# Kernel tuning notes

Hardware: AMD Instinct MI355X
Metric: run time of the kernel (lower is better)

Reference implementation:

```python
import jax, jax.numpy as jnp
import numpy as np

DMODEL = 1024
HEADS = 16
HEAD_SIZE = DMODEL // HEADS


def setup_inputs() -> dict:
    key = jax.random.key(0)
    ks = jax.random.split(key, 9)
    s = 1.0 / np.sqrt(DMODEL)
    x = jax.random.normal(ks[0], (4, 2048, DMODEL), dtype=jnp.float32)
    Wq = jax.random.uniform(ks[1], (DMODEL, DMODEL), jnp.float32, -s, s)
    bq = jax.random.uniform(ks[2], (DMODEL,), jnp.float32, -s, s)
    Wk = jax.random.uniform(ks[3], (DMODEL, DMODEL), jnp.float32, -s, s)
    bk = jax.random.uniform(ks[4], (DMODEL,), jnp.float32, -s, s)
    Wv = jax.random.uniform(ks[5], (DMODEL, DMODEL), jnp.float32, -s, s)
    bv = jax.random.uniform(ks[6], (DMODEL,), jnp.float32, -s, s)
    Wo = jax.random.uniform(ks[7], (DMODEL, DMODEL), jnp.float32, -s, s)
    bo = jax.random.uniform(ks[8], (DMODEL,), jnp.float32, -s, s)
    return {"x": x, "Wq": Wq, "bq": bq, "Wk": Wk, "bk": bk,
            "Wv": Wv, "bv": bv, "Wo": Wo, "bo": bo}


def _split_heads(t):
    b, s, _ = t.shape
    return t.reshape(b, s, HEADS, HEAD_SIZE).transpose(0, 2, 1, 3)  # [b,h,s,d]


def reference(x, Wq, bq, Wk, bk, Wv, bv, Wo, bo):
    q = _split_heads(x @ Wq.T + bq)
    k = _split_heads(x @ Wk.T + bk)
    v = _split_heads(x @ Wv.T + bv)
    scale = 1.0 / jnp.sqrt(jnp.float32(HEAD_SIZE))
    scores = jnp.einsum("bhqd,bhkd->bhqk", q, k) * scale  # full [B,H,S,S]
    attn = jax.nn.softmax(scores, axis=-1)
    out = jnp.einsum("bhqk,bhkd->bhqd", attn, v)
    b, h, s, d = out.shape
    out = out.transpose(0, 2, 1, 3).reshape(b, s, h * d)
    return out @ Wo.T + bo
```

## Files before the change

kernel.cpp:

```cpp
#include <hip/hip_runtime.h>

typedef _Float16 f16x8 __attribute__((ext_vector_type(8)));
typedef _Float16 f16x4 __attribute__((ext_vector_type(4)));
typedef float f32x4 __attribute__((ext_vector_type(4)));
typedef unsigned u32x2 __attribute__((ext_vector_type(2)));

#define MFMA16(a, b, c) __builtin_amdgcn_mfma_f32_16x16x32_f16(a, b, c, 0, 0, 0)

static constexpr int DM   = 1024;
static constexpr int SEQ  = 2048;
static constexpr int NHEAD = 16;
static constexpr int HD   = 64;

#if __has_builtin(__builtin_amdgcn_exp2f) && \
    __has_builtin(__builtin_amdgcn_permlane32_swap) && \
    __has_builtin(__builtin_amdgcn_permlane16_swap)
#define SAFE_CHAIN 1
#else
#define SAFE_CHAIN 0
#endif

__device__ __forceinline__ float fexp2(float x) {
#if SAFE_CHAIN
  return __builtin_amdgcn_exp2f(x);
#else
  float y; asm("v_exp_f32 %0, %1" : "=v"(y) : "v"(x)); return y;
#endif
}

__device__ __forceinline__ void plswap2(unsigned& x, unsigned& y) {
#if SAFE_CHAIN
  u32x2 r = __builtin_amdgcn_permlane32_swap(x, y, false, false);
  u32x2 r2 = __builtin_amdgcn_permlane16_swap(r[0], r[1], false, false);
  x = r2[0]; y = r2[1];
#else
  asm("v_permlane32_swap_b32 %0, %1" : "+v"(x), "+v"(y));
  asm("v_permlane16_swap_b32 %0, %1" : "+v"(x), "+v"(y));
#endif
}

#if SAFE_CHAIN
#define SM_PRIO(x)
#else
#define SM_PRIO(x) __builtin_amdgcn_s_setprio(x)
#endif

__device__ __forceinline__ void gload16(const _Float16* g, _Float16* l) {
  __builtin_amdgcn_global_load_lds((const __attribute__((address_space(1))) void*)g,
                                   (__attribute__((address_space(3))) void*)l, 16, 0, 0);
}

__global__ __launch_bounds__(256) void cvt_kernel(
    const float* __restrict__ x,  const float* __restrict__ wq,
    const float* __restrict__ wk, const float* __restrict__ wv,
    const float* __restrict__ wo, _Float16* __restrict__ dst)
{
  const int NX4 = 2097152;
  const int NW4 = 262144;
  const int total = NX4 + 4 * NW4;
  for (int i = blockIdx.x * blockDim.x + threadIdx.x; i < total;
       i += gridDim.x * blockDim.x) {
    const float* src; size_t doff; int off;
    if (i < NX4) { src = x; off = i; doff = (size_t)i * 4; }
    else {
      int j = i - NX4; int wi = j >> 18; off = j & (NW4 - 1);
      src = wi == 0 ? wq : wi == 1 ? wk : wi == 2 ? wv : wo;
      doff = 8388608u + (size_t)wi * 1048576u + (size_t)off * 4;
    }
    f32x4 v = *(const f32x4*)(src + (size_t)off * 4);
    f16x4 hh;
    hh[0] = (_Float16)v[0]; hh[1] = (_Float16)v[1];
    hh[2] = (_Float16)v[2]; hh[3] = (_Float16)v[3];
    *(f16x4*)(dst + doff) = hh;
  }
}

__device__ __forceinline__ void gemm_core(
    const _Float16* __restrict__ Abase, const _Float16* __restrict__ Bbase,
    int K, _Float16* Ls, int w, int l, int wr, int wc,
    f32x4 acc[4][4])
{
  const int l15 = l & 15, lg = l >> 4;
  const _Float16* src[4];
  int slot[4];
  #pragma unroll
  for (int j = 0; j < 4; j++) {
    int s = j * 256 + w * 64 + l;
    int row = s >> 3, cp = s & 7, c = cp ^ (row & 7);
    src[j] = (c < 4 ? Abase : Bbase) + (size_t)row * K + (c & 3) * 8;
    slot[j] = s * 8;
  }
  const int xo = (lg ^ (l15 & 7)) << 3;
  const int nsteps = K / 32;

  #define STAGE_G(k0, buf)                        \
    do {                                          \
      _Float16* d = Ls + (buf) * 8192;            \
      gload16(src[0] + (k0), d + slot[0]);        \
      gload16(src[1] + (k0), d + slot[1]);        \
      gload16(src[2] + (k0), d + slot[2]);        \
      gload16(src[3] + (k0), d + slot[3]);        \
    } while (0)

  STAGE_G(0, 0);
  asm volatile("s_waitcnt vmcnt(0)" ::: "memory");

  int cur = 0;
  for (int t = 0; t < nsteps; t++) {
    __builtin_amdgcn_s_barrier();
    asm volatile("" ::: "memory");

    if (t + 1 < nsteps) STAGE_G((t + 1) * 32, cur ^ 1);

    const _Float16* ls = Ls + cur * 8192;
    f16x8 af[4], bfr[4];
    #pragma unroll
    for (int mt = 0; mt < 4; mt++)
      af[mt] = *(const f16x8*)(ls + (wr * 64 + mt * 16 + l15) * 64 + xo);
    #pragma unroll
    for (int nt = 0; nt < 4; nt++)
      bfr[nt] = *(const f16x8*)(ls + (wc * 64 + nt * 16 + l15) * 64 + (xo ^ 32));

    __builtin_amdgcn_s_setprio(1);
    #pragma unroll
    for (int mt = 0; mt < 4; mt++)
      #pragma unroll
      for (int nt = 0; nt < 4; nt++)
        acc[mt][nt] = MFMA16(af[mt], bfr[nt], acc[mt][nt]);
    __builtin_amdgcn_s_setprio(0);

    if (t + 1 < nsteps) {
      asm volatile("s_waitcnt lgkmcnt(0)" ::: "memory");
      asm volatile("s_waitcnt vmcnt(0)" ::: "memory");
      __builtin_amdgcn_sched_barrier(0);
    }
    cur ^= 1;
  }
  #undef STAGE_G
}

__global__ __launch_bounds__(256, 4) void qkv_gemm(
    const _Float16* __restrict__ xh,
    const _Float16* __restrict__ wqh, const _Float16* __restrict__ wkh,
    const _Float16* __restrict__ wvh,
    const float* __restrict__ bq, const float* __restrict__ bk,
    const float* __restrict__ bv,
    _Float16* __restrict__ qo, _Float16* __restrict__ ko,
    _Float16* __restrict__ vto)
{
  __shared__ __attribute__((aligned(16))) _Float16 Ls[16384];
  const int tid = threadIdx.x, w = tid >> 6, l = tid & 63;
  const int l15 = l & 15, lg = l >> 4;
  const int wr = w >> 1, wc = w & 1;

  const int lin = blockIdx.x + blockIdx.y * 24;
  const int c = lin & 7;
  const int idx = lin >> 3;
  const int bx = c * 3 + idx % 3;
  const int m0 = (idx / 3) * 128;

  const int sel = bx >> 3;
  const int n0 = (bx & 7) * 128;
  const _Float16* W = sel == 0 ? wqh : sel == 1 ? wkh : wvh;
  const float* bias = sel == 0 ? bq : sel == 1 ? bk : bv;

  f32x4 acc[4][4] = {};
  gemm_core(xh + (size_t)m0 * DM, W + (size_t)n0 * DM, DM, Ls, w, l, wr, wc, acc);

  float biasv[4];
  #pragma unroll
  for (int nt = 0; nt < 4; nt++) biasv[nt] = bias[n0 + wc * 64 + nt * 16 + l15];

  if (sel < 2) {
    _Float16* outp = sel == 0 ? qo : ko;
    #pragma unroll
    for (int mt = 0; mt < 4; mt++) {
      int row = m0 + wr * 64 + mt * 16 + lg * 4;
      #pragma unroll
      for (int nt = 0; nt < 4; nt++) {
        int col = n0 + wc * 64 + nt * 16 + l15;
        #pragma unroll
        for (int r = 0; r < 4; r++)
          outp[(size_t)(row + r) * DM + col] = (_Float16)(acc[mt][nt][r] + biasv[nt]);
      }
    }
  } else {
    #pragma unroll
    for (int mt = 0; mt < 4; mt++) {
      int row0 = m0 + wr * 64 + mt * 16 + lg * 4;
      int b = row0 >> 11, s0 = row0 & 2047;
      #pragma unroll
      for (int nt = 0; nt < 4; nt++) {
        int col = n0 + wc * 64 + nt * 16 + l15;
        int hh = col >> 6, d = col & 63;
        f16x4 pk;
        #pragma unroll
        for (int r = 0; r < 4; r++) pk[r] = (_Float16)(acc[mt][nt][r] + biasv[nt]);
        *(f16x4*)(vto + ((size_t)((b * NHEAD + hh) * HD + d)) * SEQ + s0) = pk;
      }
    }
  }
}

__global__ __launch_bounds__(256, 3) void attn_kernel(
    const _Float16* __restrict__ qh, const _Float16* __restrict__ kh,
    const _Float16* __restrict__ vth, _Float16* __restrict__ atth)
{
  __shared__ __attribute__((aligned(16))) _Float16 Ks[2][4096];
  __shared__ __attribute__((aligned(16))) _Float16 Vs[2][4096];

  const int gid = blockIdx.x;
  const int bh = gid & 63, qt = gid >> 6;
  const int b = bh >> 4, h = bh & 15;
  const int tid = threadIdx.x, w = tid >> 6, l = tid & 63;
  const int l15 = l & 15, lg = l >> 4;
  const int q0 = qt * 128 + w * 32;

  const float c2 = 0.125f * 1.4426950408889634f;
  const _Float16 hc2 = (_Float16)c2;

  const _Float16* qbase = qh + (size_t)(b * SEQ + q0) * DM + h * HD;
  f16x8 aq[2][2];
  #pragma unroll
  for (int g = 0; g < 2; g++)
    #pragma unroll
    for (int ks = 0; ks < 2; ks++) {
      f16x8 v = *(const f16x8*)(qbase + (size_t)(g * 16 + l15) * DM + ks * 32 + lg * 8);
      #pragma unroll
      for (int j = 0; j < 8; j++) v[j] *= hc2;
      aq[g][ks] = v;
    }

  const _Float16* kbase = kh + (size_t)b * SEQ * DM + h * HD;
  const _Float16* vbase = vth + (size_t)bh * HD * SEQ;

  const int s0 = w * 64 + l, s1 = 256 + s0;
  const int kr0 = s0 >> 3, kc0 = (s0 & 7) ^ (kr0 & 7);
  const int kr1 = s1 >> 3, kc1 = (s1 & 7) ^ (kr1 & 7);

  #define STAGE_A(kv, buf)                                                        \
    do {                                                                          \
      gload16(kbase + (size_t)((kv) + kr0) * DM + kc0 * 8, &Ks[buf][s0 * 8]);     \
      gload16(kbase + (size_t)((kv) + kr1) * DM + kc1 * 8, &Ks[buf][s1 * 8]);     \
      gload16(vbase + (size_t)kr0 * SEQ + (kv) + kc0 * 8, &Vs[buf][s0 * 8]);      \
      gload16(vbase + (size_t)kr1 * SEQ + (kv) + kc1 * 8, &Vs[buf][s1 * 8]);      \
    } while (0)

  f32x4 o[2][4] = {};
  f32x4 lr[2] = {};
  f16x8 ones;
  #pragma unroll
  for (int j = 0; j < 8; j++) ones[j] = (_Float16)1.0f;

  STAGE_A(0, 0);
  asm volatile("s_waitcnt vmcnt(0)" ::: "memory");

  int cur = 0;
  for (int t = 0; t < 32; t++) {
    __builtin_amdgcn_s_barrier();
    asm volatile("" ::: "memory");

    if (t < 31) STAGE_A((t + 1) * 64, cur ^ 1);

    const _Float16* kb = &Ks[cur][0];
    f16x8 bkf[4][2];
    #pragma unroll
    for (int nt = 0; nt < 4; nt++)
      #pragma unroll
      for (int ks = 0; ks < 2; ks++)
        bkf[nt][ks] = *(const f16x8*)&kb[(nt * 16 + l15) * 64 + (((ks * 4 + lg) ^ (l15 & 7)) << 3)];

    f16x8 pa[2][2];
    #pragma unroll
    for (int g = 0; g < 2; g++) {
      f32x4 sc[4] = {};
      SM_PRIO(1);
      #pragma unroll
      for (int nt = 0; nt < 4; nt++) {
        sc[nt] = MFMA16(bkf[nt][0], aq[g][0], sc[nt]);
        sc[nt] = MFMA16(bkf[nt][1], aq[g][1], sc[nt]);
      }
      SM_PRIO(0);

      unsigned pkA[4], pkB[4];
      #pragma unroll
      for (int nt = 0; nt < 4; nt++) {
        float e0 = fexp2(sc[nt][0]), e1 = fexp2(sc[nt][1]);
        float e2 = fexp2(sc[nt][2]), e3 = fexp2(sc[nt][3]);
        pkA[nt] = __builtin_bit_cast(unsigned, __builtin_amdgcn_cvt_pkrtz(e0, e1));
        pkB[nt] = __builtin_bit_cast(unsigned, __builtin_amdgcn_cvt_pkrtz(e2, e3));
      }
      #pragma unroll
      for (int ks = 0; ks < 2; ks++) {
        unsigned a0 = pkA[2 * ks], a1 = pkA[2 * ks + 1];
        unsigned b0 = pkB[2 * ks], b1 = pkB[2 * ks + 1];
        plswap2(a0, a1);
        plswap2(b0, b1);
        union { unsigned u[4]; f16x8 v; } pk;
        pk.u[0] = a0; pk.u[1] = b0; pk.u[2] = a1; pk.u[3] = b1;
        pa[g][ks] = pk.v;
      }
    }

    const _Float16* vb = &Vs[cur][0];
    f16x8 vf[4][2];
    #pragma unroll
    for (int nt = 0; nt < 4; nt++)
      #pragma unroll
      for (int ks = 0; ks < 2; ks++)
        vf[nt][ks] = *(const f16x8*)&vb[(nt * 16 + l15) * 64 + (((ks * 4 + lg) ^ (l15 & 7)) << 3)];

    SM_PRIO(1);
    #pragma unroll
    for (int g = 0; g < 2; g++) {
      lr[g] = MFMA16(pa[g][0], ones, lr[g]);
      lr[g] = MFMA16(pa[g][1], ones, lr[g]);
      #pragma unroll
      for (int nt = 0; nt < 4; nt++) {
        o[g][nt] = MFMA16(pa[g][0], vf[nt][0], o[g][nt]);
        o[g][nt] = MFMA16(pa[g][1], vf[nt][1], o[g][nt]);
      }
    }
    SM_PRIO(0);

    if (t < 31) {
      asm volatile("s_waitcnt lgkmcnt(0)" ::: "memory");
      asm volatile("s_waitcnt vmcnt(0)" ::: "memory");
      __builtin_amdgcn_sched_barrier(0);
    }
    cur ^= 1;
  }
  #undef STAGE_A

  #pragma unroll
  for (int g = 0; g < 2; g++)
    #pragma unroll
    for (int r = 0; r < 4; r++) {
      float inv = 1.f / lr[g][r];
      int row = q0 + g * 16 + lg * 4 + r;
      #pragma unroll
      for (int nt = 0; nt < 4; nt++)
        atth[(size_t)(b * SEQ + row) * DM + h * HD + nt * 16 + l15] =
            (_Float16)(o[g][nt][r] * inv);
    }
}

__global__ __launch_bounds__(256, 4) void out_gemm(
    const _Float16* __restrict__ ah, const _Float16* __restrict__ woh,
    const float* __restrict__ bo, float* __restrict__ out)
{
  __shared__ __attribute__((aligned(16))) _Float16 Ls[16384];
  const int tid = threadIdx.x, w = tid >> 6, l = tid & 63;
  const int l15 = l & 15, lg = l >> 4;
  const int wr = w >> 1, wc = w & 1;
  const int n0 = blockIdx.x * 128;
  const int m0 = blockIdx.y * 128;

  f32x4 acc[4][4] = {};
  gemm_core(ah + (size_t)m0 * DM, woh + (size_t)n0 * DM, DM, Ls, w, l, wr, wc, acc);

  float biasv[4];
  #pragma unroll
  for (int nt = 0; nt < 4; nt++) biasv[nt] = bo[n0 + wc * 64 + nt * 16 + l15];
  #pragma unroll
  for (int mt = 0; mt < 4; mt++) {
    int row = m0 + wr * 64 + mt * 16 + lg * 4;
    #pragma unroll
    for (int nt = 0; nt < 4; nt++) {
      int col = n0 + wc * 64 + nt * 16 + l15;
      #pragma unroll
      for (int r = 0; r < 4; r++)
        out[(size_t)(row + r) * DM + col] = acc[mt][nt][r] + biasv[nt];
    }
  }
}

extern "C" void kernel_launch(void* const* d_in, const int* in_sizes, int n_in,
                              void* d_out, int out_size, void* d_ws, size_t ws_size,
                              hipStream_t stream)
{
  const float* x  = (const float*)d_in[0];
  const float* Wq = (const float*)d_in[1];
  const float* bq = (const float*)d_in[2];
  const float* Wk = (const float*)d_in[3];
  const float* bk = (const float*)d_in[4];
  const float* Wv = (const float*)d_in[5];
  const float* bv = (const float*)d_in[6];
  const float* Wo = (const float*)d_in[7];
  const float* bo = (const float*)d_in[8];
  float* out = (float*)d_out;

  _Float16* base = (_Float16*)d_ws;
  _Float16* xh  = base;
  _Float16* wqh = base + 8388608;
  _Float16* wkh = base + 9437184;
  _Float16* wvh = base + 10485760;
  _Float16* woh = base + 11534336;
  _Float16* qhp = base + 12582912;
  _Float16* khp = base + 20971520;
  _Float16* vth = base + 29360128;
  _Float16* ath = xh;

  cvt_kernel<<<1024, 256, 0, stream>>>(x, Wq, Wk, Wv, Wo, base);
  qkv_gemm<<<dim3(24, 64), 256, 0, stream>>>(xh, wqh, wkh, wvh, bq, bk, bv, qhp, khp, vth);
  attn_kernel<<<1024, 256, 0, stream>>>(qhp, khp, vth, ath);
  out_gemm<<<dim3(8, 64), 256, 0, stream>>>(ath, woh, bo, out);
}
```

Baseline: 178.2 us.

## Halve attention query tile per block and double grid size

Each attention wave now handles 16 query rows instead of 32, so a block covers 64 queries and the grid doubles to 2048 blocks. This raises the number of blocks and lowers per-wave register pressure, which may help occupancy and load balance. The cost is that every K/V tile loaded into shared memory is reused by half as many queries, doubling K/V global traffic and staging work. The set-priority calls are also made unconditional instead of compiled out on the builtin path.

```diff
diff --git a/kernel.cpp b/kernel.cpp
--- a/kernel.cpp
+++ b/kernel.cpp
@@ -38,12 +38,6 @@
   asm("v_permlane16_swap_b32 %0, %1" : "+v"(x), "+v"(y));
 #endif
 }
-
-#if SAFE_CHAIN
-#define SM_PRIO(x)
-#else
-#define SM_PRIO(x) __builtin_amdgcn_s_setprio(x)
-#endif
 
 __device__ __forceinline__ void gload16(const _Float16* g, _Float16* l) {
   __builtin_amdgcn_global_load_lds((const __attribute__((address_space(1))) void*)g,
@@ -214,22 +208,20 @@
   const int b = bh >> 4, h = bh & 15;
   const int tid = threadIdx.x, w = tid >> 6, l = tid & 63;
   const int l15 = l & 15, lg = l >> 4;
-  const int q0 = qt * 128 + w * 32;
+  const int q0 = qt * 64 + w * 16;
 
   const float c2 = 0.125f * 1.4426950408889634f;
   const _Float16 hc2 = (_Float16)c2;
 
   const _Float16* qbase = qh + (size_t)(b * SEQ + q0) * DM + h * HD;
-  f16x8 aq[2][2];
-  #pragma unroll
-  for (int g = 0; g < 2; g++)
-    #pragma unroll
-    for (int ks = 0; ks < 2; ks++) {
-      f16x8 v = *(const f16x8*)(qbase + (size_t)(g * 16 + l15) * DM + ks * 32 + lg * 8);
-      #pragma unroll
-      for (int j = 0; j < 8; j++) v[j] *= hc2;
-      aq[g][ks] = v;
-    }
+  f16x8 aq[2];
+  #pragma unroll
+  for (int ks = 0; ks < 2; ks++) {
+    f16x8 v = *(const f16x8*)(qbase + (size_t)l15 * DM + ks * 32 + lg * 8);
+    #pragma unroll
+    for (int j = 0; j < 8; j++) v[j] *= hc2;
+    aq[ks] = v;
+  }
 
   const _Float16* kbase = kh + (size_t)b * SEQ * DM + h * HD;
   const _Float16* vbase = vth + (size_t)bh * HD * SEQ;
@@ -246,8 +238,8 @@
       gload16(vbase + (size_t)kr1 * SEQ + (kv) + kc1 * 8, &Vs[buf][s1 * 8]);      \
     } while (0)
 
-  f32x4 o[2][4] = {};
-  f32x4 lr[2] = {};
+  f32x4 o[4] = {};
+  f32x4 lr = {};
   f16x8 ones;
   #pragma unroll
   for (int j = 0; j < 8; j++) ones[j] = (_Float16)1.0f;
@@ -270,37 +262,14 @@
       for (int ks = 0; ks < 2; ks++)
         bkf[nt][ks] = *(const f16x8*)&kb[(nt * 16 + l15) * 64 + (((ks * 4 + lg) ^ (l15 & 7)) << 3)];
 
-    f16x8 pa[2][2];
-    #pragma unroll
-    for (int g = 0; g < 2; g++) {
-      f32x4 sc[4] = {};
-      SM_PRIO(1);
-      #pragma unroll
-      for (int nt = 0; nt < 4; nt++) {
-        sc[nt] = MFMA16(bkf[nt][0], aq[g][0], sc[nt]);
-        sc[nt] = MFMA16(bkf[nt][1], aq[g][1], sc[nt]);
-      }
-      SM_PRIO(0);
-
-      unsigned pkA[4], pkB[4];
-      #pragma unroll
-      for (int nt = 0; nt < 4; nt++) {
-        float e0 = fexp2(sc[nt][0]), e1 = fexp2(sc[nt][1]);
-        float e2 = fexp2(sc[nt][2]), e3 = fexp2(sc[nt][3]);
-        pkA[nt] = __builtin_bit_cast(unsigned, __builtin_amdgcn_cvt_pkrtz(e0, e1));
-        pkB[nt] = __builtin_bit_cast(unsigned, __builtin_amdgcn_cvt_pkrtz(e2, e3));
-      }
-      #pragma unroll
-      for (int ks = 0; ks < 2; ks++) {
-        unsigned a0 = pkA[2 * ks], a1 = pkA[2 * ks + 1];
-        unsigned b0 = pkB[2 * ks], b1 = pkB[2 * ks + 1];
-        plswap2(a0, a1);
-        plswap2(b0, b1);
-        union { unsigned u[4]; f16x8 v; } pk;
-        pk.u[0] = a0; pk.u[1] = b0; pk.u[2] = a1; pk.u[3] = b1;
-        pa[g][ks] = pk.v;
-      }
-    }
+    f32x4 sc[4] = {};
+    __builtin_amdgcn_s_setprio(1);
+    #pragma unroll
+    for (int nt = 0; nt < 4; nt++) {
+      sc[nt] = MFMA16(bkf[nt][0], aq[0], sc[nt]);
+      sc[nt] = MFMA16(bkf[nt][1], aq[1], sc[nt]);
+    }
+    __builtin_amdgcn_s_setprio(0);
 
     const _Float16* vb = &Vs[cur][0];
     f16x8 vf[4][2];
@@ -310,18 +279,35 @@
       for (int ks = 0; ks < 2; ks++)
         vf[nt][ks] = *(const f16x8*)&vb[(nt * 16 + l15) * 64 + (((ks * 4 + lg) ^ (l15 & 7)) << 3)];
 
-    SM_PRIO(1);
-    #pragma unroll
-    for (int g = 0; g < 2; g++) {
-      lr[g] = MFMA16(pa[g][0], ones, lr[g]);
-      lr[g] = MFMA16(pa[g][1], ones, lr[g]);
-      #pragma unroll
-      for (int nt = 0; nt < 4; nt++) {
-        o[g][nt] = MFMA16(pa[g][0], vf[nt][0], o[g][nt]);
-        o[g][nt] = MFMA16(pa[g][1], vf[nt][1], o[g][nt]);
-      }
-    }
-    SM_PRIO(0);
+    unsigned pkA[4], pkB[4];
+    #pragma unroll
+    for (int nt = 0; nt < 4; nt++) {
+      float e0 = fexp2(sc[nt][0]), e1 = fexp2(sc[nt][1]);
+      float e2 = fexp2(sc[nt][2]), e3 = fexp2(sc[nt][3]);
+      pkA[nt] = __builtin_bit_cast(unsigned, __builtin_amdgcn_cvt_pkrtz(e0, e1));
+      pkB[nt] = __builtin_bit_cast(unsigned, __builtin_amdgcn_cvt_pkrtz(e2, e3));
+    }
+    f16x8 pa[2];
+    #pragma unroll
+    for (int ks = 0; ks < 2; ks++) {
+      unsigned a0 = pkA[2 * ks], a1 = pkA[2 * ks + 1];
+      unsigned b0 = pkB[2 * ks], b1 = pkB[2 * ks + 1];
+      plswap2(a0, a1);
+      plswap2(b0, b1);
+      union { unsigned u[4]; f16x8 v; } pk;
+      pk.u[0] = a0; pk.u[1] = b0; pk.u[2] = a1; pk.u[3] = b1;
+      pa[ks] = pk.v;
+    }
+
+    __builtin_amdgcn_s_setprio(1);
+    lr = MFMA16(pa[0], ones, lr);
+    lr = MFMA16(pa[1], ones, lr);
+    #pragma unroll
+    for (int nt = 0; nt < 4; nt++) {
+      o[nt] = MFMA16(pa[0], vf[nt][0], o[nt]);
+      o[nt] = MFMA16(pa[1], vf[nt][1], o[nt]);
+    }
+    __builtin_amdgcn_s_setprio(0);
 
     if (t < 31) {
       asm volatile("s_waitcnt lgkmcnt(0)" ::: "memory");
@@ -333,16 +319,14 @@
   #undef STAGE_A
 
   #pragma unroll
-  for (int g = 0; g < 2; g++)
-    #pragma unroll
-    for (int r = 0; r < 4; r++) {
-      float inv = 1.f / lr[g][r];
-      int row = q0 + g * 16 + lg * 4 + r;
-      #pragma unroll
-      for (int nt = 0; nt < 4; nt++)
-        atth[(size_t)(b * SEQ + row) * DM + h * HD + nt * 16 + l15] =
-            (_Float16)(o[g][nt][r] * inv);
-    }
+  for (int r = 0; r < 4; r++) {
+    float inv = 1.f / lr[r];
+    int row = q0 + lg * 4 + r;
+    #pragma unroll
+    for (int nt = 0; nt < 4; nt++)
+      atth[(size_t)(b * SEQ + row) * DM + h * HD + nt * 16 + l15] =
+          (_Float16)(o[nt][r] * inv);
+  }
 }
 
 __global__ __launch_bounds__(256, 4) void out_gemm(
@@ -403,6 +387,6 @@
 
   cvt_kernel<<<1024, 256, 0, stream>>>(x, Wq, Wk, Wv, Wo, base);
   qkv_gemm<<<dim3(24, 64), 256, 0, stream>>>(xh, wqh, wkh, wvh, bq, bk, bv, qhp, khp, vth);
-  attn_kernel<<<1024, 256, 0, stream>>>(qhp, khp, vth, ath);
+  attn_kernel<<<2048, 256, 0, stream>>>(qhp, khp, vth, ath);
   out_gemm<<<dim3(8, 64), 256, 0, stream>>>(ath, woh, bo, out);
 }
```

Result: slower. 190.2 us (+6.7%).
